# Kernel optimization log

Measured on AMD Instinct MI355X. Metric: run time of the kernel, lower is better.

## Reference

```python
import jax, jax.numpy as jnp
import numpy as np

ROPE_BASE = 10000.0

def apply_rope(x):
    # x: [B, S, H, Dh]  (rotate-half / NeoX convention)
    B, S, H, Dh = x.shape
    inv_freq = 1.0 / (ROPE_BASE ** (jnp.arange(0, Dh, 2, dtype=jnp.float32) / Dh))  # [Dh/2]
    ang = jnp.arange(S, dtype=jnp.float32)[:, None] * inv_freq[None, :]             # [S, Dh/2]
    cos = jnp.cos(ang)[None, :, None, :].astype(x.dtype)  # [1,S,1,Dh/2]
    sin = jnp.sin(ang)[None, :, None, :].astype(x.dtype)
    x1, x2 = jnp.split(x, 2, axis=-1)
    return jnp.concatenate([x1 * cos - x2 * sin, x1 * sin + x2 * cos], axis=-1)

def setup_inputs() -> dict:
    key = jax.random.key(0)
    k1, k2, k3 = jax.random.split(key, 3)
    B, S, D = 2, 2048, 1024
    x = jax.random.normal(k1, (B, S, D), dtype=jnp.float32)
    attn_mask = jnp.ones((B, S), dtype=bool)
    qkv_w = jax.random.normal(k2, (D, 3 * D), dtype=jnp.float32) * (1.0 / np.sqrt(D))
    out_w = jax.random.normal(k3, (D, D), dtype=jnp.float32) * (1.0 / np.sqrt(D))
    return {"x": x, "qkv_w": qkv_w, "out_w": out_w, "attn_mask": attn_mask, "is_causal": 1}

def reference(x, qkv_w, out_w, attn_mask, is_causal):
    B, S, D = x.shape
    H = 16
    Dh = D // H
    qkv = x @ qkv_w                                  # [B,S,3D]
    q, k, v = jnp.split(qkv, 3, axis=-1)
    q = apply_rope(q.reshape(B, S, H, Dh))           # [B,S,H,Dh]
    k = apply_rope(k.reshape(B, S, H, Dh))
    v = v.reshape(B, S, H, Dh)
    scale = 1.0 / np.sqrt(Dh)
    att = jnp.einsum('bqhd,bkhd->bhqk', q, k) * scale  # [B,H,S,S]
    if is_causal:
        mask = jnp.tril(jnp.ones((S, S), dtype=bool))[None, None]
    else:
        mask = attn_mask[:, None, None, :]             # [B,1,1,S]
    att = jnp.where(mask, att, jnp.finfo(att.dtype).min)
    p = jax.nn.softmax(att, axis=-1)
    y = jnp.einsum('bhqk,bkhd->bqhd', p, v).reshape(B, S, D)
    return y @ out_w
```

## Files before the change

### kernel.cpp

```cpp
#include <hip/hip_runtime.h>
#include <hip/hip_bf16.h>

#define BB 2
#define SS 2048
#define DD 1024
#define HH 16
#define N3 3072

typedef __attribute__((ext_vector_type(8))) short bf16x8;
typedef __attribute__((ext_vector_type(4))) float f32x4;
typedef __attribute__((ext_vector_type(2))) unsigned int u32x2;

__device__ __forceinline__ float b2f(unsigned short u) {
    return __uint_as_float(((unsigned int)u) << 16);
}
__device__ __forceinline__ unsigned short f2b(float f) {
    unsigned int x = __float_as_uint(f);
    x += 0x7fffu + ((x >> 16) & 1u);
    return (unsigned short)(x >> 16);
}
__device__ __forceinline__ unsigned int pack2bf(float a, float b) {
    __hip_bfloat162 h = __float22bfloat162_rn(make_float2(a, b));
    return *(unsigned int*)&h;
}
__device__ __forceinline__ void storeC(float* p, float v) { *p = v; }
__device__ __forceinline__ void storeC(unsigned short* p, float v) { *p = f2b(v); }

__device__ __forceinline__ void gload_lds16(const void* g, void* l) {
    __builtin_amdgcn_global_load_lds(
        (__attribute__((address_space(1))) void*)g,
        (__attribute__((address_space(3))) void*)l, 16, 0, 0);
}

__global__ __launch_bounds__(256) void sincos_tab(float2* __restrict__ tab) {
    int i = blockIdx.x * 256 + threadIdx.x;
    int t = i & 31;
    int s = i >> 5;
    float inv = powf(10000.0f, -(float)t * (1.0f / 32.0f));
    float sn, c;
    sincosf((float)s * inv, &sn, &c);
    tab[i] = make_float2(c, sn);
}

__global__ __launch_bounds__(256) void cast_f32_bf16(
    const float* __restrict__ src, unsigned short* __restrict__ dst)
{
    int i = (blockIdx.x * 256 + threadIdx.x) * 4;
    float4 f = *(const float4*)(src + i);
    uint2 o;
    o.x = pack2bf(f.x, f.y);
    o.y = pack2bf(f.z, f.w);
    *(uint2*)(dst + i) = o;
}

__global__ __launch_bounds__(256) void cast_transpose(
    const float* __restrict__ src, unsigned short* __restrict__ dst,
    int R, int C)
{
    __shared__ unsigned short tile[64][66];
    const int t = threadIdx.x;
    const int c0 = blockIdx.x * 64, r0 = blockIdx.y * 64;
    const int lr = t >> 4;
    const int lc = (t & 15) * 4;
    #pragma unroll
    for (int i = 0; i < 4; ++i) {
        float4 f = *(const float4*)(src + (size_t)(r0 + lr + i * 16) * C + c0 + lc);
        tile[lr + i * 16][lc + 0] = f2b(f.x);
        tile[lr + i * 16][lc + 1] = f2b(f.y);
        tile[lr + i * 16][lc + 2] = f2b(f.z);
        tile[lr + i * 16][lc + 3] = f2b(f.w);
    }
    __syncthreads();
    #pragma unroll
    for (int i = 0; i < 4; ++i) {
        const int wr = lr + i * 16;
        ushort4 o;
        o.x = tile[lc + 0][wr];
        o.y = tile[lc + 1][wr];
        o.z = tile[lc + 2][wr];
        o.w = tile[lc + 3][wr];
        *(ushort4*)(dst + (size_t)(c0 + wr) * R + r0 + lc) = o;
    }
}

template <typename OutT, int TN>
__global__ __launch_bounds__(256) void gemm_mfma(
    const unsigned short* __restrict__ A,
    const unsigned short* __restrict__ Bt,
    OutT* __restrict__ C,
    int M, int N, int K)
{
    constexpr int NI = TN / 32;
    constexpr int NB = TN / 64;
    __shared__ unsigned short Al[128 * 32];
    __shared__ unsigned short Bl[TN * 32];
    const int tid  = threadIdx.x;
    const int wave = tid >> 6;
    const int lane = tid & 63;
    const int quad = lane >> 4;
    const int l16  = lane & 15;
    const int m0 = blockIdx.y * 128;
    const int n0 = blockIdx.x * TN;
    const int wm = (wave >> 1) * 64;
    const int wn = (wave & 1) * (TN / 2);

    const int srowA = wave * 32 + (lane >> 2);
    const int srowB = wave * (16 * NB) + (lane >> 2);
    const int scol  = (lane & 3) * 8;
    const unsigned short* gA = A  + (size_t)(m0 + srowA) * K + scol;
    const unsigned short* gB = Bt + (size_t)(n0 + srowB) * K + scol;

    f32x4 acc[4][NI];
    #pragma unroll
    for (int mi = 0; mi < 4; ++mi)
        #pragma unroll
        for (int ni = 0; ni < NI; ++ni)
            acc[mi][ni] = (f32x4){0.f, 0.f, 0.f, 0.f};

    for (int k0 = 0; k0 < K; k0 += 32) {
        __syncthreads();
        #pragma unroll
        for (int i = 0; i < 2; ++i)
            gload_lds16(gA + (size_t)i * 16 * K + k0, Al + (wave * 2 + i) * 512);
        #pragma unroll
        for (int i = 0; i < NB; ++i)
            gload_lds16(gB + (size_t)i * 16 * K + k0, Bl + (wave * NB + i) * 512);
        __syncthreads();

        bf16x8 af[4], bfr[NI];
        #pragma unroll
        for (int mi = 0; mi < 4; ++mi)
            af[mi] = *(const bf16x8*)&Al[(wm + mi * 16 + l16) * 32 + quad * 8];
        #pragma unroll
        for (int ni = 0; ni < NI; ++ni)
            bfr[ni] = *(const bf16x8*)&Bl[(wn + ni * 16 + l16) * 32 + quad * 8];
        #pragma unroll
        for (int mi = 0; mi < 4; ++mi)
            #pragma unroll
            for (int ni = 0; ni < NI; ++ni)
                acc[mi][ni] = __builtin_amdgcn_mfma_f32_16x16x32_bf16(
                    af[mi], bfr[ni], acc[mi][ni], 0, 0, 0);
    }

    #pragma unroll
    for (int mi = 0; mi < 4; ++mi) {
        #pragma unroll
        for (int r = 0; r < 4; ++r) {
            const size_t base = (size_t)(m0 + wm + mi * 16 + quad * 4 + r) * N + n0 + wn;
            #pragma unroll
            for (int ni = 0; ni < NI; ++ni)
                storeC(&C[base + ni * 16 + l16], acc[mi][ni][r]);
        }
    }
}

__global__ __launch_bounds__(256) void rope_split(
    const unsigned short* __restrict__ qkv,
    const float2* __restrict__ tab,
    unsigned short* __restrict__ qo,
    unsigned short* __restrict__ ko,
    unsigned short* __restrict__ vt)
{
    __shared__ unsigned short Vtile[64][72];

    const float SC = 0.18033688011112042f;
    const int s0 = blockIdx.x * 64;
    const int h  = blockIdx.y;
    const int b  = blockIdx.z;
    const int tid = threadIdx.x;
    const int sl = tid >> 2;
    const int qu = tid & 3;
    const size_t bh = (size_t)b * HH + h;

    const unsigned short* row = qkv + (size_t)(b * SS + s0 + sl) * N3 + h * 64;

    uint4 a0 = *(const uint4*)(row + qu * 8);
    uint4 a1 = *(const uint4*)(row + 32 + qu * 8);
    uint4 b0 = *(const uint4*)(row + DD + qu * 8);
    uint4 b1 = *(const uint4*)(row + DD + 32 + qu * 8);
    uint4 c0 = *(const uint4*)(row + 2 * DD + qu * 8);
    uint4 c1 = *(const uint4*)(row + 2 * DD + 32 + qu * 8);

    float2 cs[8];
    {
        const float4* tp = (const float4*)(tab + (size_t)(s0 + sl) * 32 + qu * 8);
        #pragma unroll
        for (int i = 0; i < 4; ++i) {
            float4 f = tp[i];
            cs[2 * i]     = make_float2(f.x, f.y);
            cs[2 * i + 1] = make_float2(f.z, f.w);
        }
    }

    const unsigned short* pa0 = (const unsigned short*)&a0;
    const unsigned short* pa1 = (const unsigned short*)&a1;
    const unsigned short* pb0 = (const unsigned short*)&b0;
    const unsigned short* pb1 = (const unsigned short*)&b1;
    const unsigned short* pc0 = (const unsigned short*)&c0;
    const unsigned short* pc1 = (const unsigned short*)&c1;

    unsigned short oq1[8], oq2[8], ok1[8], ok2[8];
    #pragma unroll
    for (int j = 0; j < 8; ++j) {
        float c = cs[j].x, sn = cs[j].y;
        float q1 = b2f(pa0[j]), q2 = b2f(pa1[j]);
        float k1 = b2f(pb0[j]), k2 = b2f(pb1[j]);
        oq1[j] = f2b((q1 * c - q2 * sn) * SC);
        oq2[j] = f2b((q1 * sn + q2 * c) * SC);
        ok1[j] = f2b(k1 * c - k2 * sn);
        ok2[j] = f2b(k1 * sn + k2 * c);
        Vtile[qu * 8 + j][sl]      = pc0[j];
        Vtile[32 + qu * 8 + j][sl] = pc1[j];
    }
    const size_t qoff = (bh * SS + s0 + sl) * 64;
    *(uint4*)(qo + qoff + qu * 8)      = *(const uint4*)oq1;
    *(uint4*)(qo + qoff + 32 + qu * 8) = *(const uint4*)oq2;
    *(uint4*)(ko + qoff + qu * 8)      = *(const uint4*)ok1;
    *(uint4*)(ko + qoff + 32 + qu * 8) = *(const uint4*)ok2;

    __syncthreads();

    const int dr = tid >> 2;
    const int ch = tid & 3;
    uint4 t0 = *(const uint4*)&Vtile[dr][ch * 16];
    uint4 t1 = *(const uint4*)&Vtile[dr][ch * 16 + 8];
    unsigned short* vrow = vt + (bh * 64 + dr) * SS + s0 + ch * 16;
    *(uint4*)vrow       = t0;
    *(uint4*)(vrow + 8) = t1;
}

__device__ __forceinline__ void attn_step(
    const unsigned short* __restrict__ Kb,
    const unsigned short* __restrict__ Vb,
    const bf16x8 qf0, const bf16x8 qf1, const bf16x8 onesf,
    f32x4 O[4], f32x4& l_acc,
    bool diag, const unsigned char* mrow,
    int kt, int quad, int l16, int csw, int qg)
{
    f32x4 Sf[4];
    #pragma unroll
    for (int st = 0; st < 4; ++st) {
        const unsigned short* kr = &Kb[(st * 16 + l16) * 64];
        bf16x8 kf0 = *(const bf16x8*)(kr + csw * 8);
        bf16x8 kf1 = *(const bf16x8*)(kr + (csw ^ 4) * 8);
        f32x4 s = (f32x4){0.f, 0.f, 0.f, 0.f};
        s = __builtin_amdgcn_mfma_f32_16x16x32_bf16(kf0, qf0, s, 0, 0, 0);
        s = __builtin_amdgcn_mfma_f32_16x16x32_bf16(kf1, qf1, s, 0, 0, 0);
        Sf[st] = s;
    }

    if (diag) {
        #pragma unroll
        for (int st = 0; st < 4; ++st) {
            const int kb0 = kt * 64 + st * 16 + quad * 4;
            #pragma unroll
            for (int r = 0; r < 4; ++r)
                if (kb0 + r > qg) Sf[st][r] = -1e30f;
        }
    } else if (mrow) {
        #pragma unroll
        for (int st = 0; st < 4; ++st) {
            uchar4 mv = *(const uchar4*)(mrow + st * 16 + quad * 4);
            if (!mv.x) Sf[st][0] = -1e30f;
            if (!mv.y) Sf[st][1] = -1e30f;
            if (!mv.z) Sf[st][2] = -1e30f;
            if (!mv.w) Sf[st][3] = -1e30f;
        }
    }

    #pragma unroll
    for (int st = 0; st < 4; ++st)
        #pragma unroll
        for (int r = 0; r < 4; ++r)
            Sf[st][r] = exp2f(Sf[st][r]);

    unsigned int W[4][2];
    #pragma unroll
    for (int st = 0; st < 4; ++st) {
        W[st][0] = pack2bf(Sf[st][0], Sf[st][1]);
        W[st][1] = pack2bf(Sf[st][2], Sf[st][3]);
    }

    unsigned int pw0[4], pw1[4];
    #pragma unroll
    for (int j = 0; j < 2; ++j) {
        u32x2 s1 = __builtin_amdgcn_permlane32_swap(W[0][j], W[1][j], false, false);
        u32x2 s2 = __builtin_amdgcn_permlane16_swap(s1.x, s1.y, false, false);
        pw0[j]     = s2.x;
        pw0[j + 2] = s2.y;
        u32x2 t1 = __builtin_amdgcn_permlane32_swap(W[2][j], W[3][j], false, false);
        u32x2 t2 = __builtin_amdgcn_permlane16_swap(t1.x, t1.y, false, false);
        pw1[j]     = t2.x;
        pw1[j + 2] = t2.y;
    }
    bf16x8 pf0 = *(const bf16x8*)pw0;
    bf16x8 pf1 = *(const bf16x8*)pw1;

    l_acc = __builtin_amdgcn_mfma_f32_16x16x32_bf16(onesf, pf0, l_acc, 0, 0, 0);
    l_acc = __builtin_amdgcn_mfma_f32_16x16x32_bf16(onesf, pf1, l_acc, 0, 0, 0);

    #pragma unroll
    for (int st = 0; st < 4; ++st) {
        const unsigned short* vr = &Vb[(st * 16 + l16) * 64];
        bf16x8 vf0 = *(const bf16x8*)(vr + csw * 8);
        bf16x8 vf1 = *(const bf16x8*)(vr + (csw ^ 4) * 8);
        O[st] = __builtin_amdgcn_mfma_f32_16x16x32_bf16(vf0, pf0, O[st], 0, 0, 0);
        O[st] = __builtin_amdgcn_mfma_f32_16x16x32_bf16(vf1, pf1, O[st], 0, 0, 0);
    }
}

__global__ __launch_bounds__(256) void flash_attn(
    const unsigned short* __restrict__ q,
    const unsigned short* __restrict__ k,
    const unsigned short* __restrict__ vt,
    unsigned short* __restrict__ y,
    const int* __restrict__ is_causal,
    const unsigned char* __restrict__ attn_mask)
{
    __shared__ unsigned short Kl[2][64 * 64];
    __shared__ unsigned short Vl[2][64 * 64];

    const int bid  = blockIdx.x;
    const int work = ((bid & 7) << 7) | (bid >> 3);
    const int bhi  = work >> 5;
    const int p    = work & 31;
    int tile;
    switch (bhi & 3) {
        case 0:  tile = p;             break;
        case 1:  tile = 31 - p;        break;
        case 2:  tile = (p + 16) & 31; break;
        default: tile = (47 - p) & 31; break;
    }
    const int b = bhi >> 4;
    const int h = bhi & 15;

    const int tid  = threadIdx.x;
    const int wave = tid >> 6;
    const int lane = tid & 63;
    const int quad = lane >> 4;
    const int l16  = lane & 15;

    const size_t bh = (size_t)b * HH + h;
    const bool causal = (is_causal[0] != 0);
    const int NT = SS / 64;
    const int ntrips = causal ? (tile + 1) : NT;

    const unsigned short* qrow = q + (bh * SS + tile * 64 + wave * 16 + l16) * 64;
    const bf16x8 qf0 = *(const bf16x8*)(qrow + quad * 8);
    const bf16x8 qf1 = *(const bf16x8*)(qrow + 32 + quad * 8);

    bf16x8 onesf;
    #pragma unroll
    for (int i = 0; i < 8; ++i) onesf[i] = (short)0x3F80;

    const unsigned short* kbase  = k  + bh * SS * 64;
    const unsigned short* vtbase = vt + bh * 64 * SS;

    const int Rl  = lane >> 3;
    const int cph = lane & 7;
    const int csw = quad ^ (l16 & 7);

    f32x4 O[4];
    #pragma unroll
    for (int st = 0; st < 4; ++st) O[st] = (f32x4){0.f, 0.f, 0.f, 0.f};
    f32x4 l_acc = (f32x4){0.f, 0.f, 0.f, 0.f};

    const int qg = tile * 64 + wave * 16 + l16;

    auto stage = [&](int kt) {
        const int buf = kt & 1;
        #pragma unroll
        for (int i = 0; i < 2; ++i) {
            const int jj = wave * 2 + i;
            const int R  = jj * 8 + Rl;
            const int cl = cph ^ (R & 7);
            gload_lds16(kbase + ((size_t)(kt * 64 + R) * 64 + cl * 8),
                        &Kl[buf][jj * 512]);
            gload_lds16(vtbase + ((size_t)R * SS + kt * 64 + cl * 8),
                        &Vl[buf][jj * 512]);
        }
    };

    stage(0);
    for (int kt = 0; kt < ntrips; ++kt) {
        __syncthreads();
        if (kt + 1 < ntrips) stage(kt + 1);

        const unsigned char* mrow = causal ? nullptr
                                           : (attn_mask + (size_t)b * SS + kt * 64);
        attn_step(Kl[kt & 1], Vl[kt & 1], qf0, qf1, onesf, O, l_acc,
                  causal && kt == tile, mrow, kt, quad, l16, csw, qg);
    }

    const float inv = 1.0f / l_acc[0];
    unsigned short* yrow = y + ((size_t)b * SS + qg) * DD + h * 64;
    #pragma unroll
    for (int st = 0; st < 4; ++st) {
        uint2 o;
        o.x = pack2bf(O[st][0] * inv, O[st][1] * inv);
        o.y = pack2bf(O[st][2] * inv, O[st][3] * inv);
        *(uint2*)(yrow + st * 16 + quad * 4) = o;
    }
}

extern "C" void kernel_launch(void* const* d_in, const int* in_sizes, int n_in,
                              void* d_out, int out_size, void* d_ws, size_t ws_size,
                              hipStream_t stream) {
    const float* x      = (const float*)d_in[0];
    const float* qkv_w  = (const float*)d_in[1];
    const float* out_w  = (const float*)d_in[2];
    const unsigned char* mask = (const unsigned char*)d_in[3];
    const int*   is_c   = (const int*)d_in[4];
    float* out = (float*)d_out;

    unsigned short* xb  = (unsigned short*)d_ws;
    unsigned short* w1t = xb  + (size_t)4096 * 1024;
    unsigned short* w2t = w1t + (size_t)3072 * 1024;
    unsigned short* qkv = w2t + (size_t)1024 * 1024;
    unsigned short* qb  = qkv + (size_t)4096 * 3072;
    unsigned short* kb  = qb  + (size_t)BB * HH * SS * 64;
    unsigned short* vt  = kb  + (size_t)BB * HH * SS * 64;
    float2* tab = (float2*)(vt + (size_t)BB * HH * SS * 64);
    unsigned short* yb = xb;

    sincos_tab<<<(SS * 32) / 256, 256, 0, stream>>>(tab);
    cast_f32_bf16<<<(4096 * 1024) / 1024, 256, 0, stream>>>(x, xb);
    cast_transpose<<<dim3(N3 / 64, DD / 64), 256, 0, stream>>>(qkv_w, w1t, DD, N3);
    cast_transpose<<<dim3(DD / 64, DD / 64), 256, 0, stream>>>(out_w, w2t, DD, DD);

    gemm_mfma<unsigned short, 128><<<dim3(N3 / 128, 4096 / 128), 256, 0, stream>>>(
        xb, w1t, qkv, 4096, N3, DD);

    rope_split<<<dim3(SS / 64, HH, BB), 256, 0, stream>>>(qkv, tab, qb, kb, vt);

    flash_attn<<<dim3(BB * HH * (SS / 64)), 256, 0, stream>>>(qb, kb, vt, yb, is_c, mask);

    gemm_mfma<float, 64><<<dim3(DD / 64, 4096 / 128), 256, 0, stream>>>(
        yb, w2t, out, 4096, DD, DD);
}
```

Before: 207.7 us.

## Shrink flash-attention blocks to 32 query rows and drop double-buffered K/V staging

The attention kernel now runs 128-thread blocks covering 32 query rows instead of 256-thread blocks covering 64, which doubles the grid. Blocks are scheduled longest-first (descending query tile) to balance the causal triangle. K/V staging goes from a double-buffered prefetch to a single buffer loaded synchronously each step with two barriers. This halves LDS per block so more blocks fit per CU, but it gives up the load/compute overlap and makes each K/V tile get loaded by twice as many blocks.

```diff
diff --git a/kernel.cpp b/kernel.cpp
--- a/kernel.cpp
+++ b/kernel.cpp
@@ -309,7 +309,7 @@
     }
 }
 
-__global__ __launch_bounds__(256) void flash_attn(
+__global__ __launch_bounds__(128) void flash_attn(
     const unsigned short* __restrict__ q,
     const unsigned short* __restrict__ k,
     const unsigned short* __restrict__ vt,
@@ -317,20 +317,13 @@
     const int* __restrict__ is_causal,
     const unsigned char* __restrict__ attn_mask)
 {
-    __shared__ unsigned short Kl[2][64 * 64];
-    __shared__ unsigned short Vl[2][64 * 64];
+    __shared__ unsigned short Kl[64 * 64];
+    __shared__ unsigned short Vl[64 * 64];
 
     const int bid  = blockIdx.x;
-    const int work = ((bid & 7) << 7) | (bid >> 3);
-    const int bhi  = work >> 5;
-    const int p    = work & 31;
-    int tile;
-    switch (bhi & 3) {
-        case 0:  tile = p;             break;
-        case 1:  tile = 31 - p;        break;
-        case 2:  tile = (p + 16) & 31; break;
-        default: tile = (47 - p) & 31; break;
-    }
+    const int work = ((bid & 7) << 8) | (bid >> 3);
+    const int bhi  = work >> 6;
+    const int j    = 63 - (work & 63);
     const int b = bhi >> 4;
     const int h = bhi & 15;
 
@@ -343,9 +336,10 @@
     const size_t bh = (size_t)b * HH + h;
     const bool causal = (is_causal[0] != 0);
     const int NT = SS / 64;
-    const int ntrips = causal ? (tile + 1) : NT;
-
-    const unsigned short* qrow = q + (bh * SS + tile * 64 + wave * 16 + l16) * 64;
+    const int tW = j >> 1;
+    const int ntrips = causal ? (tW + 1) : NT;
+
+    const unsigned short* qrow = q + (bh * SS + j * 32 + wave * 16 + l16) * 64;
     const bf16x8 qf0 = *(const bf16x8*)(qrow + quad * 8);
     const bf16x8 qf1 = *(const bf16x8*)(qrow + 32 + quad * 8);
 
@@ -365,31 +359,30 @@
     for (int st = 0; st < 4; ++st) O[st] = (f32x4){0.f, 0.f, 0.f, 0.f};
     f32x4 l_acc = (f32x4){0.f, 0.f, 0.f, 0.f};
 
-    const int qg = tile * 64 + wave * 16 + l16;
+    const int qg = j * 32 + wave * 16 + l16;
 
     auto stage = [&](int kt) {
-        const int buf = kt & 1;
-        #pragma unroll
-        for (int i = 0; i < 2; ++i) {
-            const int jj = wave * 2 + i;
+        #pragma unroll
+        for (int i = 0; i < 4; ++i) {
+            const int jj = wave * 4 + i;
             const int R  = jj * 8 + Rl;
             const int cl = cph ^ (R & 7);
             gload_lds16(kbase + ((size_t)(kt * 64 + R) * 64 + cl * 8),
-                        &Kl[buf][jj * 512]);
+                        &Kl[jj * 512]);
             gload_lds16(vtbase + ((size_t)R * SS + kt * 64 + cl * 8),
-                        &Vl[buf][jj * 512]);
+                        &Vl[jj * 512]);
         }
     };
 
-    stage(0);
     for (int kt = 0; kt < ntrips; ++kt) {
         __syncthreads();
-        if (kt + 1 < ntrips) stage(kt + 1);
+        stage(kt);
+        __syncthreads();
 
         const unsigned char* mrow = causal ? nullptr
                                            : (attn_mask + (size_t)b * SS + kt * 64);
-        attn_step(Kl[kt & 1], Vl[kt & 1], qf0, qf1, onesf, O, l_acc,
-                  causal && kt == tile, mrow, kt, quad, l16, csw, qg);
+        attn_step(Kl, Vl, qf0, qf1, onesf, O, l_acc,
+                  causal && kt == tW, mrow, kt, quad, l16, csw, qg);
     }
 
     const float inv = 1.0f / l_acc[0];
@@ -433,7 +426,7 @@
 
     rope_split<<<dim3(SS / 64, HH, BB), 256, 0, stream>>>(qkv, tab, qb, kb, vt);
 
-    flash_attn<<<dim3(BB * HH * (SS / 64)), 256, 0, stream>>>(qb, kb, vt, yb, is_c, mask);
+    flash_attn<<<dim3(BB * HH * (SS / 32)), 128, 0, stream>>>(qb, kb, vt, yb, is_c, mask);
 
     gemm_mfma<float, 64><<<dim3(DD / 64, 4096 / 128), 256, 0, stream>>>(
         yb, w2t, out, 4096, DD, DD);
```

Measured after the change: 217.7 us. 1.05x slower.

## Split long causal query tiles across two blocks and merge partials with atomics

Applied to the files above, without the earlier changes.

Causal query tiles 16..31 are split into two KV ranges, each handled by its own block. This gives 48 work items per (batch, head) with a bounded per-block trip count, to reduce tail imbalance. The split halves accumulate unnormalized O and row sums into a zeroed fp32 buffer, which reuses the dead qkv workspace, via atomicAdd. A separate merge kernel then normalizes the sums and writes bf16 output. This adds two extra launches, atomic traffic and fp32 partial reads and writes in exchange for a shorter critical path per block.

```diff
diff --git a/kernel.cpp b/kernel.cpp
--- a/kernel.cpp
+++ b/kernel.cpp
@@ -229,6 +229,11 @@
     *(uint4*)(vrow + 8) = t1;
 }
 
+__global__ __launch_bounds__(256) void zero_partials(float* __restrict__ p) {
+    int i = (blockIdx.x * 256 + threadIdx.x) * 4;
+    *(float4*)(p + i) = make_float4(0.f, 0.f, 0.f, 0.f);
+}
+
 __device__ __forceinline__ void attn_step(
     const unsigned short* __restrict__ Kb,
     const unsigned short* __restrict__ Vb,
@@ -314,6 +319,8 @@
     const unsigned short* __restrict__ k,
     const unsigned short* __restrict__ vt,
     unsigned short* __restrict__ y,
+    float* __restrict__ pO,
+    float* __restrict__ pL,
     const int* __restrict__ is_causal,
     const unsigned char* __restrict__ attn_mask)
 {
@@ -321,18 +328,22 @@
     __shared__ unsigned short Vl[2][64 * 64];
 
     const int bid  = blockIdx.x;
-    const int work = ((bid & 7) << 7) | (bid >> 3);
-    const int bhi  = work >> 5;
-    const int p    = work & 31;
-    int tile;
-    switch (bhi & 3) {
-        case 0:  tile = p;             break;
-        case 1:  tile = 31 - p;        break;
-        case 2:  tile = (p + 16) & 31; break;
-        default: tile = (47 - p) & 31; break;
-    }
+    const int work = (bid & 7) * 192 + (bid >> 3);
+    const int bhi  = work / 48;
+    const int s    = work % 48;
     const int b = bhi >> 4;
     const int h = bhi & 15;
+    const bool causal = (is_causal[0] != 0);
+
+    int tile, k0t, k1t;
+    bool split;
+    if (s < 16) {
+        tile = 16 + s; k0t = 0; k1t = 15; split = true;
+    } else {
+        const int r = s - 16, p = r >> 1;
+        if (r & 1) { tile = 15 - p; k0t = 0;  k1t = causal ? tile : 31; split = false; }
+        else       { tile = 31 - p; k0t = 16; k1t = causal ? tile : 31; split = true;  }
+    }
 
     const int tid  = threadIdx.x;
     const int wave = tid >> 6;
@@ -341,11 +352,9 @@
     const int l16  = lane & 15;
 
     const size_t bh = (size_t)b * HH + h;
-    const bool causal = (is_causal[0] != 0);
-    const int NT = SS / 64;
-    const int ntrips = causal ? (tile + 1) : NT;
-
-    const unsigned short* qrow = q + (bh * SS + tile * 64 + wave * 16 + l16) * 64;
+
+    const int qg = tile * 64 + wave * 16 + l16;
+    const unsigned short* qrow = q + (bh * SS + qg) * 64;
     const bf16x8 qf0 = *(const bf16x8*)(qrow + quad * 8);
     const bf16x8 qf1 = *(const bf16x8*)(qrow + 32 + quad * 8);
 
@@ -364,8 +373,6 @@
     #pragma unroll
     for (int st = 0; st < 4; ++st) O[st] = (f32x4){0.f, 0.f, 0.f, 0.f};
     f32x4 l_acc = (f32x4){0.f, 0.f, 0.f, 0.f};
-
-    const int qg = tile * 64 + wave * 16 + l16;
 
     auto stage = [&](int kt) {
         const int buf = kt & 1;
@@ -381,10 +388,10 @@
         }
     };
 
-    stage(0);
-    for (int kt = 0; kt < ntrips; ++kt) {
+    stage(k0t);
+    for (int kt = k0t; kt <= k1t; ++kt) {
         __syncthreads();
-        if (kt + 1 < ntrips) stage(kt + 1);
+        if (kt + 1 <= k1t) stage(kt + 1);
 
         const unsigned char* mrow = causal ? nullptr
                                            : (attn_mask + (size_t)b * SS + kt * 64);
@@ -392,15 +399,48 @@
                   causal && kt == tile, mrow, kt, quad, l16, csw, qg);
     }
 
-    const float inv = 1.0f / l_acc[0];
-    unsigned short* yrow = y + ((size_t)b * SS + qg) * DD + h * 64;
-    #pragma unroll
-    for (int st = 0; st < 4; ++st) {
-        uint2 o;
-        o.x = pack2bf(O[st][0] * inv, O[st][1] * inv);
-        o.y = pack2bf(O[st][2] * inv, O[st][3] * inv);
-        *(uint2*)(yrow + st * 16 + quad * 4) = o;
-    }
+    if (!split) {
+        const float inv = 1.0f / l_acc[0];
+        unsigned short* yrow = y + ((size_t)b * SS + qg) * DD + h * 64;
+        #pragma unroll
+        for (int st = 0; st < 4; ++st) {
+            uint2 o;
+            o.x = pack2bf(O[st][0] * inv, O[st][1] * inv);
+            o.y = pack2bf(O[st][2] * inv, O[st][3] * inv);
+            *(uint2*)(yrow + st * 16 + quad * 4) = o;
+        }
+    } else {
+        float* ob = pO + (((bh * 16 + (size_t)(tile - 16)) * 64 + wave * 16 + l16) * 64);
+        #pragma unroll
+        for (int st = 0; st < 4; ++st)
+            #pragma unroll
+            for (int r = 0; r < 4; ++r)
+                atomicAdd(ob + st * 16 + quad * 4 + r, O[st][r]);
+        if (quad == 0)
+            atomicAdd(pL + (bh * 16 + (size_t)(tile - 16)) * 64 + wave * 16 + l16,
+                      l_acc[0]);
+    }
+}
+
+__global__ __launch_bounds__(256) void attn_merge(
+    const float* __restrict__ pO, const float* __restrict__ pL,
+    unsigned short* __restrict__ y)
+{
+    const int i = (blockIdx.x * 256 + threadIdx.x) * 4;
+    float4 o = *(const float4*)(pO + i);
+    const int rowi = i >> 6;
+    const int d    = i & 63;
+    const float inv = 1.0f / pL[rowi];
+    const int row = rowi & 63;
+    const int tt  = (rowi >> 6) & 15;
+    const int bh  = rowi >> 10;
+    const int b = bh >> 4, h = bh & 15;
+    const int sq = (16 + tt) * 64 + row;
+    unsigned short* yp = y + ((size_t)b * SS + sq) * DD + h * 64 + d;
+    uint2 ov;
+    ov.x = pack2bf(o.x * inv, o.y * inv);
+    ov.y = pack2bf(o.z * inv, o.w * inv);
+    *(uint2*)yp = ov;
 }
 
 extern "C" void kernel_launch(void* const* d_in, const int* in_sizes, int n_in,
@@ -423,6 +463,9 @@
     float2* tab = (float2*)(vt + (size_t)BB * HH * SS * 64);
     unsigned short* yb = xb;
 
+    float* pO = (float*)qkv;
+    float* pL = pO + (size_t)32 * 16 * 64 * 64;
+
     sincos_tab<<<(SS * 32) / 256, 256, 0, stream>>>(tab);
     cast_f32_bf16<<<(4096 * 1024) / 1024, 256, 0, stream>>>(x, xb);
     cast_transpose<<<dim3(N3 / 64, DD / 64), 256, 0, stream>>>(qkv_w, w1t, DD, N3);
@@ -433,7 +476,12 @@
 
     rope_split<<<dim3(SS / 64, HH, BB), 256, 0, stream>>>(qkv, tab, qb, kb, vt);
 
-    flash_attn<<<dim3(BB * HH * (SS / 64)), 256, 0, stream>>>(qb, kb, vt, yb, is_c, mask);
+    zero_partials<<<2080, 256, 0, stream>>>(pO);
+
+    flash_attn<<<dim3(48 * BB * HH), 256, 0, stream>>>(qb, kb, vt, yb, pO, pL,
+                                                       is_c, mask);
+
+    attn_merge<<<2048, 256, 0, stream>>>(pO, pL, yb);
 
     gemm_mfma<float, 64><<<dim3(DD / 64, 4096 / 128), 256, 0, stream>>>(
         yb, w2t, out, 4096, DD, DD);
```

Result: slower. 233.8 us (+12.5%).
